# Kernel tuning notes

Measured on AMD Instinct MI355X. Metric: run time of the kernel, lower is better.

The kernel has to match this reference:

```python
import jax, jax.numpy as jnp
import numpy as np

D = 768      # model dim
H = 12       # heads
L = 6        # depth
B = 4        # batch
N = 1024     # tokens
MLP = 4      # mlp mult
DH = D // H  # head dim
EPS = 1e-5


def setup_inputs() -> dict:
    key = jax.random.key(0)
    ks = jax.random.split(key, 10)
    s = 0.02
    return {
        "x": jax.random.normal(ks[0], (B, N, D), jnp.float32),
        "spatial_weights": jax.random.normal(ks[1], (B, N, N), jnp.float32) * s,
        "ln1_g": jnp.ones((L, 1, 1, D), jnp.float32),
        "ln1_b": jnp.zeros((L, 1, 1, D), jnp.float32),
        "w_qkv": jax.random.normal(ks[2], (L, D, 3 * D), jnp.float32) * s,
        "w_out": jax.random.normal(ks[3], (L, D, D), jnp.float32) * s,
        "b_out": jnp.zeros((L, D), jnp.float32),
        "ln2_g": jnp.ones((L, 1, 1, D), jnp.float32),
        "ln2_b": jnp.zeros((L, 1, 1, D), jnp.float32),
        "w1": jax.random.normal(ks[4], (L, D, MLP * D), jnp.float32) * s,
        "b1": jnp.zeros((L, MLP * D), jnp.float32),
        "w2": jax.random.normal(ks[5], (L, MLP * D, D), jnp.float32) * s,
        "b2": jnp.zeros((L, D), jnp.float32),
    }


def _layer_norm(x, g, b):
    m = jnp.mean(x, axis=-1, keepdims=True)
    v = jnp.var(x, axis=-1, keepdims=True)  # biased, matches torch unbiased=False
    return (x - m) / jnp.sqrt(v + EPS) * g + b


def _attn(xn, sw, w_qkv, w_out, b_out):
    scale = DH ** -0.5
    qkv = xn @ w_qkv                                   # [b,n,3D]
    q, k, v = jnp.split(qkv, 3, axis=-1)
    def heads(t):  # 'b n (h d) -> h b n d'
        b, n, _ = t.shape
        return jnp.transpose(t.reshape(b, n, H, DH), (2, 0, 1, 3))
    q, k, v = heads(q), heads(k), heads(v)
    dots = jnp.einsum('hbid,hbjd->hbij', q, k) * scale
    dots = dots + sw[None]                             # spatial bias broadcast over heads
    attn = jax.nn.softmax(dots, axis=-1)
    out = jnp.einsum('hbij,hbjd->hbid', attn, v)
    out = jnp.transpose(out, (1, 2, 0, 3)).reshape(xn.shape[0], xn.shape[1], D)
    return out @ w_out + b_out


def reference(x, spatial_weights, ln1_g, ln1_b, w_qkv, w_out, b_out, ln2_g, ln2_b, w1, b1, w2, b2):
    for l in range(L):
        xn = _layer_norm(x, ln1_g[l], ln1_b[l])
        x = _attn(xn, spatial_weights, w_qkv[l], w_out[l], b_out[l]) + x
        xn = _layer_norm(x, ln2_g[l], ln2_b[l])
        h = jax.nn.gelu(xn @ w1[l] + b1[l], approximate=False)
        x = h @ w2[l] + b2[l] + x
    return x
```

## Files before the change

### kernel.cpp

```cpp
#include <hip/hip_runtime.h>
#include <hip/hip_bf16.h>

typedef __attribute__((ext_vector_type(8))) short short8;
typedef __attribute__((ext_vector_type(4))) float f32x4;

#define MFMA16(a, b, c) __builtin_amdgcn_mfma_f32_16x16x32_bf16(a, b, c, 0, 0, 0)

static __device__ __forceinline__ float gelu_f(float v) {
    return 0.5f * v * (1.0f + erff(v * 0.70710678118654752f));
}

__global__ __launch_bounds__(256) void ln_kernel(
    const float* __restrict__ x, const float* __restrict__ g, const float* __restrict__ bb,
    __hip_bfloat16* __restrict__ xn) {
    int row = blockIdx.x;
    const float* xr = x + (size_t)row * 768;
    int tid = threadIdx.x;
    float v0 = xr[tid], v1 = xr[tid + 256], v2 = xr[tid + 512];
    float s = v0 + v1 + v2;
    float s2 = v0 * v0 + v1 * v1 + v2 * v2;
    for (int m = 1; m < 64; m <<= 1) { s += __shfl_xor(s, m); s2 += __shfl_xor(s2, m); }
    __shared__ float ls[4], ls2[4];
    if ((tid & 63) == 0) { ls[tid >> 6] = s; ls2[tid >> 6] = s2; }
    __syncthreads();
    s = ls[0] + ls[1] + ls[2] + ls[3];
    s2 = ls2[0] + ls2[1] + ls2[2] + ls2[3];
    float mean = s * (1.0f / 768.0f);
    float var = s2 * (1.0f / 768.0f) - mean * mean;
    float rstd = rsqrtf(var + 1e-5f);
    __hip_bfloat16* xo = xn + (size_t)row * 768;
    xo[tid]       = __float2bfloat16((v0 - mean) * rstd * g[tid]       + bb[tid]);
    xo[tid + 256] = __float2bfloat16((v1 - mean) * rstd * g[tid + 256] + bb[tid + 256]);
    xo[tid + 512] = __float2bfloat16((v2 - mean) * rstd * g[tid + 512] + bb[tid + 512]);
}

__global__ __launch_bounds__(256) void reduce_ln_kernel(
    const __hip_bfloat16* __restrict__ P, int SK,
    const float* __restrict__ bias, float* __restrict__ x,
    const float* __restrict__ g, const float* __restrict__ bb,
    __hip_bfloat16* __restrict__ xn) {
    const size_t MN = (size_t)4096 * 768;
    int row = blockIdx.x, tid = threadIdx.x;
    float v[3];
    float s = 0.f, s2 = 0.f;
    for (int j = 0; j < 3; j++) {
        int c = tid + j * 256;
        size_t idx = (size_t)row * 768 + c;
        float val = x[idx] + bias[c];
        for (int sk = 0; sk < SK; sk++) val += __bfloat162float(P[(size_t)sk * MN + idx]);
        x[idx] = val;
        v[j] = val;
        s += val; s2 += val * val;
    }
    for (int m = 1; m < 64; m <<= 1) { s += __shfl_xor(s, m); s2 += __shfl_xor(s2, m); }
    __shared__ float ls[4], ls2[4];
    if ((tid & 63) == 0) { ls[tid >> 6] = s; ls2[tid >> 6] = s2; }
    __syncthreads();
    s = ls[0] + ls[1] + ls[2] + ls[3];
    s2 = ls2[0] + ls2[1] + ls2[2] + ls2[3];
    float mean = s * (1.0f / 768.0f);
    float var = s2 * (1.0f / 768.0f) - mean * mean;
    float rstd = rsqrtf(var + 1e-5f);
    __hip_bfloat16* xo = xn + (size_t)row * 768;
    for (int j = 0; j < 3; j++) {
        int c = tid + j * 256;
        xo[c] = __float2bfloat16((v[j] - mean) * rstd * g[c] + bb[c]);
    }
}

__global__ __launch_bounds__(256) void reduce_out_kernel(
    const __hip_bfloat16* __restrict__ P, int SK,
    const float* __restrict__ bias, const float* __restrict__ x,
    float* __restrict__ out) {
    const size_t MN = (size_t)4096 * 768;
    int row = blockIdx.x, tid = threadIdx.x;
    for (int j = 0; j < 3; j++) {
        int c = tid + j * 256;
        size_t idx = (size_t)row * 768 + c;
        float val = x[idx] + bias[c];
        for (int sk = 0; sk < SK; sk++) val += __bfloat162float(P[(size_t)sk * MN + idx]);
        out[idx] = val;
    }
}

__global__ __launch_bounds__(256) void transpose_cast_kernel(
    const float* __restrict__ in, __hip_bfloat16* __restrict__ out, int K, int N) {
    __shared__ float tile[32][33];
    size_t off = (size_t)blockIdx.z * K * N;
    in += off; out += off;
    int n0 = blockIdx.x * 32, k0 = blockIdx.y * 32;
    int tx = threadIdx.x & 31, ty = threadIdx.x >> 5;
    for (int i = ty; i < 32; i += 8)
        tile[i][tx] = in[(size_t)(k0 + i) * N + n0 + tx];
    __syncthreads();
    for (int i = ty; i < 32; i += 8)
        out[(size_t)(n0 + i) * K + k0 + tx] = __float2bfloat16(tile[tx][i]);
}

__global__ __launch_bounds__(256) void cast_bf16_kernel(
    const float* __restrict__ in, __hip_bfloat16* __restrict__ out, int n4) {
    int i = blockIdx.x * 256 + threadIdx.x;
    if (i >= n4) return;
    float4 v = ((const float4*)in)[i];
    __hip_bfloat16* o = out + (size_t)i * 4;
    o[0] = __float2bfloat16(v.x); o[1] = __float2bfloat16(v.y);
    o[2] = __float2bfloat16(v.z); o[3] = __float2bfloat16(v.w);
}

template <int EPI>
__global__ __launch_bounds__(256) void gemm_bt_kernel(
    const __hip_bfloat16* __restrict__ A, const __hip_bfloat16* __restrict__ Bt,
    const float* __restrict__ bias,
    void* __restrict__ Cout, int M, int N, int K, int kChunk) {
    __shared__ __hip_bfloat16 As[128 * 32];
    __shared__ __hip_bfloat16 Bs[128 * 32];
    int m0 = blockIdx.y * 128, n0 = blockIdx.x * 128;
    int kStart = blockIdx.z * kChunk;
    int tid = threadIdx.x, w = tid >> 6, lane = tid & 63;
    int quad = lane >> 4, l16 = lane & 15;
    int wm = (w & 1) * 64, wn = (w >> 1) * 64;
    f32x4 acc[4][4] = {};
    for (int kt = kStart; kt < kStart + kChunk; kt += 32) {
        __syncthreads();
        for (int c = tid; c < 512; c += 256) {
            int row = c >> 2, cc = c & 3;
            __builtin_amdgcn_global_load_lds(
                (const __attribute__((address_space(1))) void*)(A + (size_t)(m0 + row) * K + kt + cc * 8),
                (__attribute__((address_space(3))) void*)(&As[c * 8]), 16, 0, 0);
        }
        for (int c = tid; c < 512; c += 256) {
            int row = c >> 2, cc = c & 3;
            __builtin_amdgcn_global_load_lds(
                (const __attribute__((address_space(1))) void*)(Bt + (size_t)(n0 + row) * K + kt + cc * 8),
                (__attribute__((address_space(3))) void*)(&Bs[c * 8]), 16, 0, 0);
        }
        __syncthreads();
        short8 af[4], bf[4];
        for (int i = 0; i < 4; i++) {
            af[i] = *(const short8*)(As + (wm + i * 16 + l16) * 32 + quad * 8);
            bf[i] = *(const short8*)(Bs + (wn + i * 16 + l16) * 32 + quad * 8);
        }
        for (int i = 0; i < 4; i++)
            for (int j = 0; j < 4; j++)
                acc[i][j] = MFMA16(af[i], bf[j], acc[i][j]);
    }
    __hip_bfloat16* Cb = (__hip_bfloat16*)Cout;
    if (EPI == 3) Cb += (size_t)blockIdx.z * M * N;
    for (int i = 0; i < 4; i++) {
        int rbase = m0 + wm + i * 16 + quad * 4;
        for (int j = 0; j < 4; j++) {
            int col = n0 + wn + j * 16 + l16;
            float bv = (EPI == 1) ? bias[col] : 0.0f;
            for (int r = 0; r < 4; r++) {
                size_t idx = (size_t)(rbase + r) * N + col;
                float v = acc[i][j][r] + bv;
                if (EPI == 1) v = gelu_f(v);
                Cb[idx] = __float2bfloat16(v);
            }
        }
    }
}

__global__ __launch_bounds__(256) void attn_kernel(
    const __hip_bfloat16* __restrict__ qkv, const __hip_bfloat16* __restrict__ swb,
    __hip_bfloat16* __restrict__ Op, float* __restrict__ lp) {
    int qt = blockIdx.x, h = blockIdx.y;
    int b = blockIdx.z >> 1, half = blockIdx.z & 1;
    int tid = threadIdx.x, w = tid >> 6, lane = tid & 63;
    int quad = lane >> 4, l16 = lane & 15;
    __shared__ __hip_bfloat16 Ks[64 * 72];
    __shared__ __hip_bfloat16 Vt[64 * 66];
    __shared__ __hip_bfloat16 Ps[128 * 66];

    short8 qf[2][2];
    for (int mt = 0; mt < 2; mt++) {
        const __hip_bfloat16* qb =
            qkv + (size_t)(b * 1024 + qt * 128 + w * 32 + mt * 16 + l16) * 2304 + h * 64;
        qf[mt][0] = *(const short8*)(qb + quad * 8);
        qf[mt][1] = *(const short8*)(qb + 32 + quad * 8);
    }
    f32x4 o[2][4] = {};
    float lsum[2][4] = {};
    const unsigned int* Pd = (const unsigned int*)Ps;
    const unsigned int* Vd = (const unsigned int*)Vt;

    for (int kt = 0; kt < 512; kt += 64) {
        __syncthreads();
        for (int c = tid; c < 512; c += 256) {
            int row = c >> 3, ch = c & 7;
            size_t gb = (size_t)(b * 1024 + half * 512 + kt + row) * 2304 + h * 64;
            float4 kv = *(const float4*)(qkv + gb + 768 + ch * 8);
            *(float4*)(Ks + row * 72 + ch * 8) = kv;
            float4 vv = *(const float4*)(qkv + gb + 1536 + ch * 8);
            const __hip_bfloat16* pv = (const __hip_bfloat16*)&vv;
            #pragma unroll
            for (int j = 0; j < 8; j++) Vt[(ch * 8 + j) * 66 + row] = pv[j];
        }
        __syncthreads();
        f32x4 s[2][4];
        for (int nt = 0; nt < 4; nt++) {
            short8 kf0 = *(const short8*)(Ks + (nt * 16 + l16) * 72 + quad * 8);
            short8 kf1 = *(const short8*)(Ks + (nt * 16 + l16) * 72 + 32 + quad * 8);
            for (int mt = 0; mt < 2; mt++) {
                f32x4 z = {0.f, 0.f, 0.f, 0.f};
                z = MFMA16(qf[mt][0], kf0, z);
                z = MFMA16(qf[mt][1], kf1, z);
                s[mt][nt] = z;
            }
        }
        for (int mt = 0; mt < 2; mt++)
            for (int r = 0; r < 4; r++) {
                int qloc = w * 32 + mt * 16 + quad * 4 + r;
                size_t swbase = ((size_t)b << 20) + (size_t)(qt * 128 + qloc) * 1024
                              + half * 512 + kt;
                float lacc = 0.f;
                #pragma unroll
                for (int nt = 0; nt < 4; nt++) {
                    float sw_ = __bfloat162float(swb[swbase + nt * 16 + l16]);
                    float p = __expf(s[mt][nt][r] * 0.125f + sw_);
                    Ps[qloc * 66 + nt * 16 + l16] = __float2bfloat16(p);
                    lacc += p;
                }
                lsum[mt][r] += lacc;
            }
        short8 vf[4][2];
        for (int dt = 0; dt < 4; dt++)
            for (int kh = 0; kh < 2; kh++) {
                union { unsigned int u[4]; short8 s8; } t;
                int base = (dt * 16 + l16) * 33 + kh * 16 + quad * 4;
                #pragma unroll
                for (int i = 0; i < 4; i++) t.u[i] = Vd[base + i];
                vf[dt][kh] = t.s8;
            }
        for (int mt = 0; mt < 2; mt++) {
            int prow = w * 32 + mt * 16 + l16;
            short8 pf[2];
            for (int kh = 0; kh < 2; kh++) {
                union { unsigned int u[4]; short8 s8; } t;
                int base = prow * 33 + kh * 16 + quad * 4;
                #pragma unroll
                for (int i = 0; i < 4; i++) t.u[i] = Pd[base + i];
                pf[kh] = t.s8;
            }
            for (int dt = 0; dt < 4; dt++) {
                o[mt][dt] = MFMA16(pf[0], vf[dt][0], o[mt][dt]);
                o[mt][dt] = MFMA16(pf[1], vf[dt][1], o[mt][dt]);
            }
        }
    }
    for (int mt = 0; mt < 2; mt++)
        for (int r = 0; r < 4; r++) {
            float lv = lsum[mt][r];
            lv += __shfl_xor(lv, 1); lv += __shfl_xor(lv, 2);
            lv += __shfl_xor(lv, 4); lv += __shfl_xor(lv, 8);
            lsum[mt][r] = lv;
        }
    __hip_bfloat16* Oh = Op + (size_t)half * 4096 * 768;
    for (int mt = 0; mt < 2; mt++)
        for (int dt = 0; dt < 4; dt++)
            for (int r = 0; r < 4; r++) {
                int row = b * 1024 + qt * 128 + w * 32 + mt * 16 + quad * 4 + r;
                Oh[(size_t)row * 768 + h * 64 + dt * 16 + l16] = __float2bfloat16(o[mt][dt][r]);
            }
    if (l16 == 0)
        for (int mt = 0; mt < 2; mt++)
            for (int r = 0; r < 4; r++) {
                int q = qt * 128 + w * 32 + mt * 16 + quad * 4 + r;
                lp[half * 49152 + (b * 12 + h) * 1024 + q] = lsum[mt][r];
            }
}

__global__ __launch_bounds__(256) void attn_merge_kernel(
    const __hip_bfloat16* __restrict__ Op, const float* __restrict__ lp,
    __hip_bfloat16* __restrict__ att) {
    int row = blockIdx.x, tid = threadIdx.x;
    int b = row >> 10, n = row & 1023;
    for (int j = 0; j < 3; j++) {
        int c = tid + j * 256;
        int h = c >> 6;
        float l0 = lp[(b * 12 + h) * 1024 + n];
        float l1 = lp[49152 + (b * 12 + h) * 1024 + n];
        size_t idx = (size_t)row * 768 + c;
        float v = (__bfloat162float(Op[idx]) + __bfloat162float(Op[(size_t)4096 * 768 + idx]))
                  / (l0 + l1);
        att[idx] = __float2bfloat16(v);
    }
}

extern "C" void kernel_launch(void* const* d_in, const int* in_sizes, int n_in,
                              void* d_out, int out_size, void* d_ws, size_t ws_size,
                              hipStream_t stream) {
    const float* x_in  = (const float*)d_in[0];
    const float* sw_in = (const float*)d_in[1];
    const float* ln1_g = (const float*)d_in[2];
    const float* ln1_b = (const float*)d_in[3];
    const float* w_qkv = (const float*)d_in[4];
    const float* w_out = (const float*)d_in[5];
    const float* b_out = (const float*)d_in[6];
    const float* ln2_g = (const float*)d_in[7];
    const float* ln2_b = (const float*)d_in[8];
    const float* w1    = (const float*)d_in[9];
    const float* b1    = (const float*)d_in[10];
    const float* w2    = (const float*)d_in[11];
    const float* b2    = (const float*)d_in[12];

    char* ws = (char*)d_ws;
    size_t off = 0;
    auto alloc = [&](size_t bytes) -> void* {
        void* p = ws + off;
        off += (bytes + 255) & ~(size_t)255;
        return p;
    };
    float*          x     = (float*)alloc((size_t)4096 * 768 * 4);
    __hip_bfloat16* xn    = (__hip_bfloat16*)alloc((size_t)4096 * 768 * 2);
    __hip_bfloat16* qkv   = (__hip_bfloat16*)alloc((size_t)4096 * 2304 * 2);
    __hip_bfloat16* att   = (__hip_bfloat16*)alloc((size_t)4096 * 768 * 2);
    __hip_bfloat16* hbuf  = (__hip_bfloat16*)alloc((size_t)4096 * 3072 * 2);
    __hip_bfloat16* swb   = (__hip_bfloat16*)alloc((size_t)4 * 1024 * 1024 * 2);
    __hip_bfloat16* wqkvT = (__hip_bfloat16*)alloc((size_t)6 * 2304 * 768 * 2);
    __hip_bfloat16* woutT = (__hip_bfloat16*)alloc((size_t)6 * 768 * 768 * 2);
    __hip_bfloat16* w1T   = (__hip_bfloat16*)alloc((size_t)6 * 3072 * 768 * 2);
    __hip_bfloat16* w2T   = (__hip_bfloat16*)alloc((size_t)6 * 768 * 3072 * 2);
    __hip_bfloat16* Pw2   = qkv;
    __hip_bfloat16* Opart = hbuf;
    float*          lpart = (float*)(hbuf + (size_t)2 * 4096 * 768);
    __hip_bfloat16* Pproj = hbuf;

    hipMemcpyAsync(x, x_in, (size_t)4096 * 768 * 4, hipMemcpyDeviceToDevice, stream);
    transpose_cast_kernel<<<dim3(2304 / 32, 768 / 32, 6), 256, 0, stream>>>(w_qkv, wqkvT, 768, 2304);
    transpose_cast_kernel<<<dim3(768 / 32, 768 / 32, 6), 256, 0, stream>>>(w_out, woutT, 768, 768);
    transpose_cast_kernel<<<dim3(3072 / 32, 768 / 32, 6), 256, 0, stream>>>(w1, w1T, 768, 3072);
    transpose_cast_kernel<<<dim3(768 / 32, 3072 / 32, 6), 256, 0, stream>>>(w2, w2T, 3072, 768);
    cast_bf16_kernel<<<dim3(4 * 1024 * 1024 / 4 / 256), 256, 0, stream>>>(sw_in, swb, 4 * 1024 * 1024 / 4);

    ln_kernel<<<4096, 256, 0, stream>>>(x, ln1_g, ln1_b, xn);
    for (int l = 0; l < 6; l++) {
        gemm_bt_kernel<0><<<dim3(2304 / 128, 4096 / 128, 1), 256, 0, stream>>>(
            xn, wqkvT + (size_t)l * 2304 * 768, nullptr, qkv, 4096, 2304, 768, 768);
        attn_kernel<<<dim3(8, 12, 8), 256, 0, stream>>>(qkv, swb, Opart, lpart);
        attn_merge_kernel<<<4096, 256, 0, stream>>>(Opart, lpart, att);
        gemm_bt_kernel<3><<<dim3(768 / 128, 4096 / 128, 4), 256, 0, stream>>>(
            att, woutT + (size_t)l * 768 * 768, nullptr, Pproj, 4096, 768, 768, 192);
        reduce_ln_kernel<<<4096, 256, 0, stream>>>(
            Pproj, 4, b_out + l * 768, x, ln2_g + l * 768, ln2_b + l * 768, xn);
        gemm_bt_kernel<1><<<dim3(3072 / 128, 4096 / 128, 1), 256, 0, stream>>>(
            xn, w1T + (size_t)l * 3072 * 768, b1 + l * 3072, hbuf, 4096, 3072, 768, 768);
        gemm_bt_kernel<3><<<dim3(768 / 128, 4096 / 128, 4), 256, 0, stream>>>(
            hbuf, w2T + (size_t)l * 768 * 3072, nullptr, Pw2, 4096, 768, 3072, 768);
        if (l < 5) {
            reduce_ln_kernel<<<4096, 256, 0, stream>>>(
                Pw2, 4, b2 + l * 768, x, ln1_g + (l + 1) * 768, ln1_b + (l + 1) * 768, xn);
        } else {
            reduce_out_kernel<<<4096, 256, 0, stream>>>(Pw2, 4, b2 + l * 768, x, (float*)d_out);
        }
    }
}
```

Measured before the change: 1.455 ms.

## Precompute exp of spatial bias, fold q scale into QKV GEMM, split attention four ways

Replaces the additive spatial bias with a precomputed exp(bias) table, so the attention kernel multiplies by it instead of adding before the exp. The 0.125 q scale moves into the QKV GEMM epilogue. Attention is split into four key partitions instead of two, with the merge kernel summing four partials. The GEMM and K tiles switch to a k-chunk-major LDS layout loaded directly with global_load_lds, meant to cut bank conflicts. The partial row sums now live in the output buffer as scratch. Without max subtraction, exp of the scores and the bias could overflow or lose precision in bf16.

Result: slower. 1.743 ms (+19.8%).

```diff
diff --git a/kernel.cpp b/kernel.cpp
--- a/kernel.cpp
+++ b/kernel.cpp
@@ -97,14 +97,14 @@
         out[(size_t)(n0 + i) * K + k0 + tx] = __float2bfloat16(tile[tx][i]);
 }
 
-__global__ __launch_bounds__(256) void cast_bf16_kernel(
+__global__ __launch_bounds__(256) void exp_bf16_kernel(
     const float* __restrict__ in, __hip_bfloat16* __restrict__ out, int n4) {
     int i = blockIdx.x * 256 + threadIdx.x;
     if (i >= n4) return;
     float4 v = ((const float4*)in)[i];
     __hip_bfloat16* o = out + (size_t)i * 4;
-    o[0] = __float2bfloat16(v.x); o[1] = __float2bfloat16(v.y);
-    o[2] = __float2bfloat16(v.z); o[3] = __float2bfloat16(v.w);
+    o[0] = __float2bfloat16(__expf(v.x)); o[1] = __float2bfloat16(__expf(v.y));
+    o[2] = __float2bfloat16(__expf(v.z)); o[3] = __float2bfloat16(__expf(v.w));
 }
 
 template <int EPI>
@@ -112,8 +112,8 @@
     const __hip_bfloat16* __restrict__ A, const __hip_bfloat16* __restrict__ Bt,
     const float* __restrict__ bias,
     void* __restrict__ Cout, int M, int N, int K, int kChunk) {
-    __shared__ __hip_bfloat16 As[128 * 32];
-    __shared__ __hip_bfloat16 Bs[128 * 32];
+    __shared__ __hip_bfloat16 As[4 * 128 * 8];
+    __shared__ __hip_bfloat16 Bs[4 * 128 * 8];
     int m0 = blockIdx.y * 128, n0 = blockIdx.x * 128;
     int kStart = blockIdx.z * kChunk;
     int tid = threadIdx.x, w = tid >> 6, lane = tid & 63;
@@ -123,22 +123,22 @@
     for (int kt = kStart; kt < kStart + kChunk; kt += 32) {
         __syncthreads();
         for (int c = tid; c < 512; c += 256) {
-            int row = c >> 2, cc = c & 3;
+            int row = c & 127, q = c >> 7;
             __builtin_amdgcn_global_load_lds(
-                (const __attribute__((address_space(1))) void*)(A + (size_t)(m0 + row) * K + kt + cc * 8),
+                (const __attribute__((address_space(1))) void*)(A + (size_t)(m0 + row) * K + kt + q * 8),
                 (__attribute__((address_space(3))) void*)(&As[c * 8]), 16, 0, 0);
         }
         for (int c = tid; c < 512; c += 256) {
-            int row = c >> 2, cc = c & 3;
+            int row = c & 127, q = c >> 7;
             __builtin_amdgcn_global_load_lds(
-                (const __attribute__((address_space(1))) void*)(Bt + (size_t)(n0 + row) * K + kt + cc * 8),
+                (const __attribute__((address_space(1))) void*)(Bt + (size_t)(n0 + row) * K + kt + q * 8),
                 (__attribute__((address_space(3))) void*)(&Bs[c * 8]), 16, 0, 0);
         }
         __syncthreads();
         short8 af[4], bf[4];
         for (int i = 0; i < 4; i++) {
-            af[i] = *(const short8*)(As + (wm + i * 16 + l16) * 32 + quad * 8);
-            bf[i] = *(const short8*)(Bs + (wn + i * 16 + l16) * 32 + quad * 8);
+            af[i] = *(const short8*)(As + quad * 1024 + (wm + i * 16 + l16) * 8);
+            bf[i] = *(const short8*)(Bs + quad * 1024 + (wn + i * 16 + l16) * 8);
         }
         for (int i = 0; i < 4; i++)
             for (int j = 0; j < 4; j++)
@@ -146,6 +146,7 @@
     }
     __hip_bfloat16* Cb = (__hip_bfloat16*)Cout;
     if (EPI == 3) Cb += (size_t)blockIdx.z * M * N;
+    float qscale = (EPI == 4 && n0 < 768) ? 0.125f : 1.0f;
     for (int i = 0; i < 4; i++) {
         int rbase = m0 + wm + i * 16 + quad * 4;
         for (int j = 0; j < 4; j++) {
@@ -155,6 +156,7 @@
                 size_t idx = (size_t)(rbase + r) * N + col;
                 float v = acc[i][j][r] + bv;
                 if (EPI == 1) v = gelu_f(v);
+                if (EPI == 4) v *= qscale;
                 Cb[idx] = __float2bfloat16(v);
             }
         }
@@ -162,13 +164,13 @@
 }
 
 __global__ __launch_bounds__(256) void attn_kernel(
-    const __hip_bfloat16* __restrict__ qkv, const __hip_bfloat16* __restrict__ swb,
+    const __hip_bfloat16* __restrict__ qkv, const __hip_bfloat16* __restrict__ E,
     __hip_bfloat16* __restrict__ Op, float* __restrict__ lp) {
     int qt = blockIdx.x, h = blockIdx.y;
-    int b = blockIdx.z >> 1, half = blockIdx.z & 1;
+    int b = blockIdx.z >> 2, part = blockIdx.z & 3;
     int tid = threadIdx.x, w = tid >> 6, lane = tid & 63;
     int quad = lane >> 4, l16 = lane & 15;
-    __shared__ __hip_bfloat16 Ks[64 * 72];
+    __shared__ __hip_bfloat16 Ks[8 * 64 * 8];
     __shared__ __hip_bfloat16 Vt[64 * 66];
     __shared__ __hip_bfloat16 Ps[128 * 66];
 
@@ -184,14 +186,19 @@
     const unsigned int* Pd = (const unsigned int*)Ps;
     const unsigned int* Vd = (const unsigned int*)Vt;
 
-    for (int kt = 0; kt < 512; kt += 64) {
+    for (int kt = 0; kt < 256; kt += 64) {
+        int key0 = part * 256 + kt;
         __syncthreads();
         for (int c = tid; c < 512; c += 256) {
+            int key = c & 63, q = c >> 6;
+            __builtin_amdgcn_global_load_lds(
+                (const __attribute__((address_space(1))) void*)(
+                    qkv + (size_t)(b * 1024 + key0 + key) * 2304 + 768 + h * 64 + q * 8),
+                (__attribute__((address_space(3))) void*)(&Ks[c * 8]), 16, 0, 0);
+        }
+        for (int c = tid; c < 512; c += 256) {
             int row = c >> 3, ch = c & 7;
-            size_t gb = (size_t)(b * 1024 + half * 512 + kt + row) * 2304 + h * 64;
-            float4 kv = *(const float4*)(qkv + gb + 768 + ch * 8);
-            *(float4*)(Ks + row * 72 + ch * 8) = kv;
-            float4 vv = *(const float4*)(qkv + gb + 1536 + ch * 8);
+            float4 vv = *(const float4*)(qkv + (size_t)(b * 1024 + key0 + row) * 2304 + 1536 + h * 64 + ch * 8);
             const __hip_bfloat16* pv = (const __hip_bfloat16*)&vv;
             #pragma unroll
             for (int j = 0; j < 8; j++) Vt[(ch * 8 + j) * 66 + row] = pv[j];
@@ -199,8 +206,8 @@
         __syncthreads();
         f32x4 s[2][4];
         for (int nt = 0; nt < 4; nt++) {
-            short8 kf0 = *(const short8*)(Ks + (nt * 16 + l16) * 72 + quad * 8);
-            short8 kf1 = *(const short8*)(Ks + (nt * 16 + l16) * 72 + 32 + quad * 8);
+            short8 kf0 = *(const short8*)(Ks + quad * 512 + (nt * 16 + l16) * 8);
+            short8 kf1 = *(const short8*)(Ks + (quad + 4) * 512 + (nt * 16 + l16) * 8);
             for (int mt = 0; mt < 2; mt++) {
                 f32x4 z = {0.f, 0.f, 0.f, 0.f};
                 z = MFMA16(qf[mt][0], kf0, z);
@@ -211,13 +218,12 @@
         for (int mt = 0; mt < 2; mt++)
             for (int r = 0; r < 4; r++) {
                 int qloc = w * 32 + mt * 16 + quad * 4 + r;
-                size_t swbase = ((size_t)b << 20) + (size_t)(qt * 128 + qloc) * 1024
-                              + half * 512 + kt;
+                size_t ebase = ((size_t)b << 20) + (size_t)(qt * 128 + qloc) * 1024 + key0;
                 float lacc = 0.f;
                 #pragma unroll
                 for (int nt = 0; nt < 4; nt++) {
-                    float sw_ = __bfloat162float(swb[swbase + nt * 16 + l16]);
-                    float p = __expf(s[mt][nt][r] * 0.125f + sw_);
+                    float e = __bfloat162float(E[ebase + nt * 16 + l16]);
+                    float p = __expf(s[mt][nt][r]) * e;
                     Ps[qloc * 66 + nt * 16 + l16] = __float2bfloat16(p);
                     lacc += p;
                 }
@@ -255,7 +261,7 @@
             lv += __shfl_xor(lv, 4); lv += __shfl_xor(lv, 8);
             lsum[mt][r] = lv;
         }
-    __hip_bfloat16* Oh = Op + (size_t)half * 4096 * 768;
+    __hip_bfloat16* Oh = Op + (size_t)part * 4096 * 768;
     for (int mt = 0; mt < 2; mt++)
         for (int dt = 0; dt < 4; dt++)
             for (int r = 0; r < 4; r++) {
@@ -266,24 +272,26 @@
         for (int mt = 0; mt < 2; mt++)
             for (int r = 0; r < 4; r++) {
                 int q = qt * 128 + w * 32 + mt * 16 + quad * 4 + r;
-                lp[half * 49152 + (b * 12 + h) * 1024 + q] = lsum[mt][r];
+                lp[part * 49152 + (b * 12 + h) * 1024 + q] = lsum[mt][r];
             }
 }
 
 __global__ __launch_bounds__(256) void attn_merge_kernel(
     const __hip_bfloat16* __restrict__ Op, const float* __restrict__ lp,
     __hip_bfloat16* __restrict__ att) {
+    const size_t MN = (size_t)4096 * 768;
     int row = blockIdx.x, tid = threadIdx.x;
     int b = row >> 10, n = row & 1023;
     for (int j = 0; j < 3; j++) {
         int c = tid + j * 256;
         int h = c >> 6;
-        float l0 = lp[(b * 12 + h) * 1024 + n];
-        float l1 = lp[49152 + (b * 12 + h) * 1024 + n];
+        float l = 0.f, v = 0.f;
         size_t idx = (size_t)row * 768 + c;
-        float v = (__bfloat162float(Op[idx]) + __bfloat162float(Op[(size_t)4096 * 768 + idx]))
-                  / (l0 + l1);
-        att[idx] = __float2bfloat16(v);
+        for (int p = 0; p < 4; p++) {
+            l += lp[p * 49152 + (b * 12 + h) * 1024 + n];
+            v += __bfloat162float(Op[p * MN + idx]);
+        }
+        att[idx] = __float2bfloat16(v / l);
     }
 }
 
@@ -316,14 +324,14 @@
     __hip_bfloat16* qkv   = (__hip_bfloat16*)alloc((size_t)4096 * 2304 * 2);
     __hip_bfloat16* att   = (__hip_bfloat16*)alloc((size_t)4096 * 768 * 2);
     __hip_bfloat16* hbuf  = (__hip_bfloat16*)alloc((size_t)4096 * 3072 * 2);
-    __hip_bfloat16* swb   = (__hip_bfloat16*)alloc((size_t)4 * 1024 * 1024 * 2);
+    __hip_bfloat16* Ebuf  = (__hip_bfloat16*)alloc((size_t)4 * 1024 * 1024 * 2);
     __hip_bfloat16* wqkvT = (__hip_bfloat16*)alloc((size_t)6 * 2304 * 768 * 2);
     __hip_bfloat16* woutT = (__hip_bfloat16*)alloc((size_t)6 * 768 * 768 * 2);
     __hip_bfloat16* w1T   = (__hip_bfloat16*)alloc((size_t)6 * 3072 * 768 * 2);
     __hip_bfloat16* w2T   = (__hip_bfloat16*)alloc((size_t)6 * 768 * 3072 * 2);
     __hip_bfloat16* Pw2   = qkv;
     __hip_bfloat16* Opart = hbuf;
-    float*          lpart = (float*)(hbuf + (size_t)2 * 4096 * 768);
+    float*          lpart = (float*)d_out;
     __hip_bfloat16* Pproj = hbuf;
 
     hipMemcpyAsync(x, x_in, (size_t)4096 * 768 * 4, hipMemcpyDeviceToDevice, stream);
@@ -331,13 +339,13 @@
     transpose_cast_kernel<<<dim3(768 / 32, 768 / 32, 6), 256, 0, stream>>>(w_out, woutT, 768, 768);
     transpose_cast_kernel<<<dim3(3072 / 32, 768 / 32, 6), 256, 0, stream>>>(w1, w1T, 768, 3072);
     transpose_cast_kernel<<<dim3(768 / 32, 3072 / 32, 6), 256, 0, stream>>>(w2, w2T, 3072, 768);
-    cast_bf16_kernel<<<dim3(4 * 1024 * 1024 / 4 / 256), 256, 0, stream>>>(sw_in, swb, 4 * 1024 * 1024 / 4);
+    exp_bf16_kernel<<<dim3(4 * 1024 * 1024 / 4 / 256), 256, 0, stream>>>(sw_in, Ebuf, 4 * 1024 * 1024 / 4);
 
     ln_kernel<<<4096, 256, 0, stream>>>(x, ln1_g, ln1_b, xn);
     for (int l = 0; l < 6; l++) {
-        gemm_bt_kernel<0><<<dim3(2304 / 128, 4096 / 128, 1), 256, 0, stream>>>(
+        gemm_bt_kernel<4><<<dim3(2304 / 128, 4096 / 128, 1), 256, 0, stream>>>(
             xn, wqkvT + (size_t)l * 2304 * 768, nullptr, qkv, 4096, 2304, 768, 768);
-        attn_kernel<<<dim3(8, 12, 8), 256, 0, stream>>>(qkv, swb, Opart, lpart);
+        attn_kernel<<<dim3(8, 12, 16), 256, 0, stream>>>(qkv, Ebuf, Opart, lpart);
         attn_merge_kernel<<<4096, 256, 0, stream>>>(Opart, lpart, att);
         gemm_bt_kernel<3><<<dim3(768 / 128, 4096 / 128, 4), 256, 0, stream>>>(
             att, woutT + (size_t)l * 768 * 768, nullptr, Pproj, 4096, 768, 768, 192);
```
